# Kernel optimization log

Measured on AMD Instinct MI355X. Metric: run time of the kernel, lower is better.

Reference implementation:

```python
import jax, jax.numpy as jnp
import numpy as np

D_MODEL = 1024
D_K = 1024
D_V = 1024
N_HEAD = 16
EPS = 1e-5
BS, N_TOK = 2, 2048


def setup_inputs() -> dict:
    key = jax.random.key(0)
    ks = jax.random.split(key, 12)
    s = 0.02
    q = jax.random.normal(ks[0], (BS, N_TOK, D_MODEL), jnp.float32)
    k = jax.random.normal(ks[1], (BS, N_TOK, D_MODEL), jnp.float32)
    v = jax.random.normal(ks[2], (BS, N_TOK, D_MODEL), jnp.float32)
    return {
        "q": q, "k": k, "v": v,
        "gamma": jnp.ones((D_MODEL,), jnp.float32),
        "beta": jnp.zeros((D_MODEL,), jnp.float32),
        "Wq": jax.random.normal(ks[3], (D_MODEL, D_K), jnp.float32) * s,
        "bq": jnp.zeros((D_K,), jnp.float32),
        "Wk": jax.random.normal(ks[4], (D_MODEL, D_K), jnp.float32) * s,
        "bk": jnp.zeros((D_K,), jnp.float32),
        "Wv": jax.random.normal(ks[5], (D_MODEL, D_V), jnp.float32) * s,
        "bv": jnp.zeros((D_V,), jnp.float32),
        "Wo": jax.random.normal(ks[6], (D_V, D_MODEL), jnp.float32) * s,
        "bo": jnp.zeros((D_MODEL,), jnp.float32),
    }


def reference(q, k, v, gamma, beta, Wq, bq, Wk, bk, Wv, bv, Wo, bo):
    # NOTE: original module ignores k, v args; self-attention over q.
    bs, n_tok, d_m = q.shape
    d_h = D_K // N_HEAD
    temper = float(np.sqrt(d_h))

    # LayerNorm1d over d_model
    mu = jnp.mean(q, axis=-1, keepdims=True)
    var = jnp.var(q, axis=-1, keepdims=True)
    h = (q - mu) / jnp.sqrt(var + EPS) * gamma + beta

    # projections; head split = chunk along feature dim -> [bs, H, T, d_h]
    qh = (h @ Wq + bq).reshape(bs, n_tok, N_HEAD, d_h).transpose(0, 2, 1, 3)
    kh = (h @ Wk + bk).reshape(bs, n_tok, N_HEAD, d_h).transpose(0, 2, 1, 3)
    vh = jax.nn.relu(h @ Wv + bv).reshape(bs, n_tok, N_HEAD, d_h).transpose(0, 2, 1, 3)

    scores = jnp.einsum('bhqd,bhkd->bhqk', qh, kh) / temper
    # dropout before softmax in train mode; identity in eval (deterministic ref)
    attn = jax.nn.softmax(scores, axis=-1)
    o = jnp.einsum('bhqk,bhkd->bhqd', attn, vh)  # [bs, H, T, d_h]

    # faithful to torch: view(bs, n_tok, -1) with NO head transpose (head-major merge)
    merged = o.reshape(bs, n_tok, N_HEAD * d_h)
    out = merged @ Wo + bo + q  # proj + residual
    return out
```

## Files before the change

### kernel.cpp

```cpp
#include <hip/hip_runtime.h>

typedef __bf16 bf16;
typedef __bf16 bf16x8 __attribute__((ext_vector_type(8)));
typedef __bf16 bf16x4 __attribute__((ext_vector_type(4)));
typedef float  f32x4  __attribute__((ext_vector_type(4)));
typedef float  f32x16 __attribute__((ext_vector_type(16)));
typedef unsigned int u32;
typedef u32 u32x4 __attribute__((ext_vector_type(4)));

#define AS1U(p) ((const __attribute__((address_space(1))) unsigned int*)(p))
#define AS3U(p) ((__attribute__((address_space(3))) unsigned int*)(p))

static __device__ __forceinline__ u32 pack2(float a, float b) {
    unsigned short ua = __builtin_bit_cast(unsigned short, (bf16)a);
    unsigned short ub = __builtin_bit_cast(unsigned short, (bf16)b);
    return (u32)ua | ((u32)ub << 16);
}

__global__ void prep_kernel(const float* __restrict__ q,
                            const float* __restrict__ gamma,
                            const float* __restrict__ beta,
                            bf16* __restrict__ h,
                            const float* __restrict__ W0, const float* __restrict__ W1,
                            const float* __restrict__ W2, const float* __restrict__ W3,
                            bf16* __restrict__ D0, bf16* __restrict__ D1,
                            bf16* __restrict__ D2, bf16* __restrict__ D3) {
    __shared__ float tile[32][33];
    __shared__ float ssum[4], ssum2[4];
    const int blk = blockIdx.x;
    const int t = threadIdx.x;
    if (blk < 4096) {
        const float* xr = q + (size_t)blk * 1024;
        float4 v = ((const float4*)xr)[t];
        float s  = v.x + v.y + v.z + v.w;
        float s2 = v.x * v.x + v.y * v.y + v.z * v.z + v.w * v.w;
#pragma unroll
        for (int m = 1; m < 64; m <<= 1) {
            s  += __shfl_xor(s, m, 64);
            s2 += __shfl_xor(s2, m, 64);
        }
        const int wid = t >> 6, lane = t & 63;
        if (lane == 0) { ssum[wid] = s; ssum2[wid] = s2; }
        __syncthreads();
        s  = ssum[0] + ssum[1] + ssum[2] + ssum[3];
        s2 = ssum2[0] + ssum2[1] + ssum2[2] + ssum2[3];
        const float mu  = s * (1.f / 1024.f);
        const float var = s2 * (1.f / 1024.f) - mu * mu;
        const float rs  = rsqrtf(var + 1e-5f);
        float4 g = ((const float4*)gamma)[t];
        float4 b = ((const float4*)beta)[t];
        bf16x4 o;
        o[0] = (bf16)((v.x - mu) * rs * g.x + b.x);
        o[1] = (bf16)((v.y - mu) * rs * g.y + b.y);
        o[2] = (bf16)((v.z - mu) * rs * g.z + b.z);
        o[3] = (bf16)((v.w - mu) * rs * g.w + b.w);
        ((bf16x4*)(h + (size_t)blk * 1024))[t] = o;
    } else {
        const int z = blk - 4096;
        const float* W; bf16* D;
        switch (z >> 10) {
            case 0: W = W0; D = D0; break;
            case 1: W = W1; D = D1; break;
            case 2: W = W2; D = D2; break;
            default: W = W3; D = D3; break;
        }
        const int bi = (z & 1023) >> 5, bj = z & 31;
        const int tx = t & 31, ty = t >> 5;
#pragma unroll
        for (int i = 0; i < 4; i++) {
            tile[ty + i * 8][tx] = W[(size_t)(bi * 32 + ty + i * 8) * 1024 + bj * 32 + tx];
        }
        __syncthreads();
#pragma unroll
        for (int i = 0; i < 4; i++) {
            D[(size_t)(bj * 32 + ty + i * 8) * 1024 + bi * 32 + tx] =
                (bf16)tile[tx][ty + i * 8];
        }
    }
}

template <int EPI>
__global__ void gemm_kernel(const bf16* __restrict__ A, const bf16* __restrict__ BT,
                            int N, int K,
                            bf16* __restrict__ Cb,
                            const float* __restrict__ b0, const float* __restrict__ b1,
                            const float* __restrict__ b2, bf16* __restrict__ Vt,
                            float* __restrict__ Cf, const float* __restrict__ bo,
                            const float* __restrict__ resid) {
    __shared__ bf16 Asm[128][32];
    __shared__ bf16 Bsm[128][32];
    const int tid = threadIdx.x;
    const int lane = tid & 63, wave = tid >> 6;
    const int wr = wave >> 1, wc = wave & 1;
    const int nwg = gridDim.x * gridDim.y;
    const int bid0 = blockIdx.y * gridDim.x + blockIdx.x;
    const int bid = (bid0 & 7) * (nwg >> 3) + (bid0 >> 3);
    const int tileN = (bid % gridDim.x) * 128;
    const int tileM = (bid / gridDim.x) * 128;
    const int row16 = lane & 15, g = lane >> 4;

    f32x4 acc[4][4] = {};

    for (int kt = 0; kt < K; kt += 32) {
#pragma unroll
        for (int i = 0; i < 2; i++) {
            int c = tid + i * 256;
            int r = c >> 2, cb = (c & 3) * 16;
            const char* g_ = (const char*)(A + (size_t)(tileM + r) * K + kt) + cb;
            char* l_ = (char*)&Asm[0][0] + c * 16;
            __builtin_amdgcn_global_load_lds(AS1U(g_), AS3U(l_), 16, 0, 0);
        }
#pragma unroll
        for (int i = 0; i < 2; i++) {
            int c = tid + i * 256;
            int r = c >> 2, cb = (c & 3) * 16;
            const char* g_ = (const char*)(BT + (size_t)(tileN + r) * K + kt) + cb;
            char* l_ = (char*)&Bsm[0][0] + c * 16;
            __builtin_amdgcn_global_load_lds(AS1U(g_), AS3U(l_), 16, 0, 0);
        }
        __syncthreads();
        bf16x8 af[4], bfr[4];
#pragma unroll
        for (int m = 0; m < 4; m++)
            af[m] = *(const bf16x8*)&Asm[wr * 64 + m * 16 + row16][g * 8];
#pragma unroll
        for (int n = 0; n < 4; n++)
            bfr[n] = *(const bf16x8*)&Bsm[wc * 64 + n * 16 + row16][g * 8];
#pragma unroll
        for (int m = 0; m < 4; m++)
#pragma unroll
            for (int n = 0; n < 4; n++)
                acc[m][n] = __builtin_amdgcn_mfma_f32_16x16x32_bf16(af[m], bfr[n],
                                                                   acc[m][n], 0, 0, 0);
        __syncthreads();
    }

    if constexpr (EPI == 0) {
        __shared__ bf16 Ep[4][64][64];
        char* ep = (char*)&Ep[wave][0][0];
        const bool isV = (tileN >= 2048);
        if (!isV) {
#pragma unroll
            for (int n = 0; n < 4; n++) {
                const int cl = n * 16 + row16;
                const int gc = tileN + wc * 64 + cl;
                const float bias = gc < 1024 ? b0[gc] : b1[gc - 1024];
                const float scl = gc < 1024 ? 0.18033688011112042f : 1.f;
#pragma unroll
                for (int m = 0; m < 4; m++)
#pragma unroll
                    for (int j = 0; j < 4; j++) {
                        const int rl = m * 16 + g * 4 + j;
                        const float v = (acc[m][n][j] + bias) * scl;
                        *(bf16*)(ep + rl * 128 + ((cl * 2) ^ ((rl & 7) << 4))) = (bf16)v;
                    }
            }
        } else {
#pragma unroll
            for (int n = 0; n < 4; n++) {
                const int dl = n * 16 + row16;
                const float bias = b2[(tileN - 2048) + wc * 64 + dl];
#pragma unroll
                for (int m = 0; m < 4; m++)
#pragma unroll
                    for (int j = 0; j < 4; j++) {
                        const int tl = m * 16 + g * 4 + j;
                        const float v = fmaxf(acc[m][n][j] + bias, 0.f);
                        *(bf16*)(ep + dl * 128 + ((tl * 2) ^ ((dl & 7) << 4))) = (bf16)v;
                    }
            }
        }
        asm volatile("s_waitcnt lgkmcnt(0)" ::: "memory");
        __builtin_amdgcn_sched_barrier(0);
        if (!isV) {
#pragma unroll
            for (int it = 0; it < 8; it++) {
                const int rl = (lane >> 3) + it * 8;
                const bf16x8 vrow = *(const bf16x8*)(ep + rl * 128 +
                                                     (((lane & 7) * 16) ^ ((rl & 7) << 4)));
                const int gr = tileM + wr * 64 + rl;
                const int gc = tileN + wc * 64 + (lane & 7) * 8;
                *(bf16x8*)&Cb[(size_t)gr * N + gc] = vrow;
            }
        } else {
            const int bb = tileM >> 11;
            const int tbase = (tileM & 2047) + wr * 64 + (lane & 7) * 8;
#pragma unroll
            for (int it = 0; it < 8; it++) {
                const int dl = (lane >> 3) + it * 8;
                const bf16x8 vrow = *(const bf16x8*)(ep + dl * 128 +
                                                     (((lane & 7) * 16) ^ ((dl & 7) << 4)));
                const int gd = (tileN - 2048) + wc * 64 + dl;
                const int hh = gd >> 6, dd = gd & 63;
                *(bf16x8*)&Vt[(((size_t)bb * 16 + hh) * 64 + dd) * 2048 + tbase] = vrow;
            }
        }
    } else {
        __shared__ float Epf[4][64][66];
        float* ep = &Epf[wave][0][0];
#pragma unroll
        for (int n = 0; n < 4; n++) {
            const int cl = n * 16 + row16;
            const float bias = bo[tileN + wc * 64 + cl];
#pragma unroll
            for (int m = 0; m < 4; m++)
#pragma unroll
                for (int j = 0; j < 4; j++) {
                    const int rl = m * 16 + g * 4 + j;
                    ep[rl * 66 + cl] = acc[m][n][j] + bias;
                }
        }
        asm volatile("s_waitcnt lgkmcnt(0)" ::: "memory");
        __builtin_amdgcn_sched_barrier(0);
        const int rl0 = lane >> 4;
        const int cl0 = (lane & 15) * 4;
#pragma unroll
        for (int it = 0; it < 16; it++) {
            const int rl = rl0 + it * 4;
            float4 v = *(const float4*)&ep[rl * 66 + cl0];
            const int gr = tileM + wr * 64 + rl;
            const int gc = tileN + wc * 64 + cl0;
            const float4 rv = *(const float4*)&resid[(size_t)gr * N + gc];
            v.x += rv.x; v.y += rv.y; v.z += rv.z; v.w += rv.w;
            *(float4*)&Cf[(size_t)gr * N + gc] = v;
        }
    }
}

__global__ __launch_bounds__(512, 4)
void attn_kernel(const bf16* __restrict__ qkv, const bf16* __restrict__ Vt,
                 bf16* __restrict__ Obuf) {
    const int bid = blockIdx.x;
    const int swz = (bid & 7) * 64 + (bid >> 3);
    const int bh = swz >> 4, qt = swz & 15;
    const int b = bh >> 4, h = bh & 15;
    const int qbase = qt * 128;
    const int tid = threadIdx.x;
    const int lane = tid & 63, wv = tid >> 6;
    const int half = wv >> 2, qw = wv & 3;
    const int c = lane & 31, p = lane >> 5;

    __shared__ bf16 Kl[2][2][64][64];
    __shared__ bf16 Vl[2][2][64][64];

    const bf16* qrow = qkv + (size_t)(b * 2048 + qbase + qw * 32 + c) * 3072 + h * 64;
    bf16x8 qf[4];
#pragma unroll
    for (int ch = 0; ch < 4; ch++)
        qf[ch] = *(const bf16x8*)(qrow + ch * 16 + p * 8);

    const char* kgbase = (const char*)(qkv + (size_t)b * 2048 * 3072 + 1024 + h * 64)
                         + (size_t)(half * 1024) * 6144;
    const char* vgbase = (const char*)(Vt + (size_t)bh * 64 * 2048) + half * 2048;
    const int ht = tid & 255;
    const char* kgp[2]; const char* vgp[2]; int ldo[2];
#pragma unroll
    for (int i = 0; i < 2; i++) {
        const int cc = ht + i * 256;
        const int srow = cc >> 3;
        const int scol = ((cc & 7) * 16) ^ ((srow & 7) << 4);
        kgp[i] = kgbase + (size_t)srow * 6144 + scol;
        vgp[i] = vgbase + (size_t)srow * 4096 + scol;
        ldo[i] = cc * 16;
    }
    char* kldb = (char*)&Kl[half][0][0][0];
    char* vldb = (char*)&Vl[half][0][0][0];

    auto stage = [&](int t, int slot) {
        const size_t ko = (size_t)t * (64 * 6144);
        const size_t vo = (size_t)t * 128;
        const int sb = slot * 8192;
#pragma unroll
        for (int i = 0; i < 2; i++) {
            __builtin_amdgcn_global_load_lds(AS1U(kgp[i] + ko), AS3U(kldb + sb + ldo[i]), 16, 0, 0);
            __builtin_amdgcn_global_load_lds(AS1U(vgp[i] + vo), AS3U(vldb + sb + ldo[i]), 16, 0, 0);
        }
    };

    f32x16 accO[2] = {};
    f32x16 accL = {};
    const f32x16 z16 = {};
    const u32 one2 = 0x3F803F80u;
    const u32x4 onesw = {one2, one2, one2, one2};
    const bf16x8 onesf = __builtin_bit_cast(bf16x8, onesw);

    auto compute = [&](int slot) {
        const char* Kb = (const char*)&Kl[half][slot][0][0];
        const char* Vb = (const char*)&Vl[half][slot][0][0];
#pragma unroll
        for (int cc = 0; cc < 2; cc++) {
            const int tok = cc * 32 + c;
            const bf16x8 kf0 = *(const bf16x8*)(Kb + tok * 128 + ((0 * 32 + p * 16) ^ ((tok & 7) << 4)));
            f32x16 accT = __builtin_amdgcn_mfma_f32_32x32x16_bf16(kf0, qf[0], z16, 0, 0, 0);
#pragma unroll
            for (int ch = 1; ch < 4; ch++) {
                const bf16x8 kf = *(const bf16x8*)(Kb + tok * 128 +
                                                   ((ch * 32 + p * 16) ^ ((tok & 7) << 4)));
                accT = __builtin_amdgcn_mfma_f32_32x32x16_bf16(kf, qf[ch], accT, 0, 0, 0);
            }
            float pv[16];
#pragma unroll
            for (int r = 0; r < 16; r++) pv[r] = exp2f(accT[r]);
            u32 k01 = pack2(pv[0], pv[1]),  k23 = pack2(pv[2], pv[3]);
            u32 k45 = pack2(pv[4], pv[5]),  k67 = pack2(pv[6], pv[7]);
            u32 k89 = pack2(pv[8], pv[9]),  kab = pack2(pv[10], pv[11]);
            u32 kcd = pack2(pv[12], pv[13]), kef = pack2(pv[14], pv[15]);
            asm("v_permlane32_swap_b32 %0, %1" : "+v"(k45), "+v"(k01));
            asm("v_permlane32_swap_b32 %0, %1" : "+v"(k67), "+v"(k23));
            asm("v_permlane32_swap_b32 %0, %1" : "+v"(kcd), "+v"(k89));
            asm("v_permlane32_swap_b32 %0, %1" : "+v"(kef), "+v"(kab));
            u32x4 w0w = {k01, k23, k45, k67};
            u32x4 w1w = {k89, kab, kcd, kef};
            const bf16x8 pf0 = __builtin_bit_cast(bf16x8, w0w);
            const bf16x8 pf1 = __builtin_bit_cast(bf16x8, w1w);
            accL = __builtin_amdgcn_mfma_f32_32x32x16_bf16(pf0, onesf, accL, 0, 0, 0);
            accL = __builtin_amdgcn_mfma_f32_32x32x16_bf16(pf1, onesf, accL, 0, 0, 0);
#pragma unroll
            for (int dc = 0; dc < 2; dc++) {
                const int rd = dc * 32 + c;
                const int sw = (rd & 7) << 4;
                const bf16x8 vf0 = *(const bf16x8*)(Vb + rd * 128 + ((cc * 64 + p * 16) ^ sw));
                const bf16x8 vf1 = *(const bf16x8*)(Vb + rd * 128 + ((cc * 64 + 32 + p * 16) ^ sw));
                accO[dc] = __builtin_amdgcn_mfma_f32_32x32x16_bf16(pf0, vf0, accO[dc], 0, 0, 0);
                accO[dc] = __builtin_amdgcn_mfma_f32_32x32x16_bf16(pf1, vf1, accO[dc], 0, 0, 0);
            }
        }
    };

#define KV_SYNC() do { \
        asm volatile("s_waitcnt vmcnt(0)" ::: "memory"); \
        __builtin_amdgcn_s_barrier(); \
        asm volatile("" ::: "memory"); \
    } while (0)

    stage(0, 0);
#pragma unroll 1
    for (int t = 0; t < 14; t += 2) {
        KV_SYNC(); stage(t + 1, 1); compute(0);
        KV_SYNC(); stage(t + 2, 0); compute(1);
    }
    KV_SYNC(); stage(15, 1); compute(0);
    KV_SYNC(); compute(1);
#undef KV_SYNC

    __syncthreads();
    float* ex = (float*)&Kl[0][0][0][0];
    const int xb = (qw * 64 + lane) * 49;
    if (half) {
#pragma unroll
        for (int dc = 0; dc < 2; dc++)
#pragma unroll
            for (int r = 0; r < 16; r++) ex[xb + dc * 16 + r] = accO[dc][r];
#pragma unroll
        for (int r = 0; r < 16; r++) ex[xb + 32 + r] = accL[r];
    }
    __syncthreads();
    if (!half) {
#pragma unroll
        for (int dc = 0; dc < 2; dc++)
#pragma unroll
            for (int r = 0; r < 16; r++) accO[dc][r] += ex[xb + dc * 16 + r];
#pragma unroll
        for (int r = 0; r < 16; r++) accL[r] += ex[xb + 32 + r];
        bf16* ob = Obuf + ((size_t)bh * 2048 + qbase + qw * 32) * 64;
#pragma unroll
        for (int r = 0; r < 16; r++) {
            const float inv = 1.f / accL[r];
            const int row = (r & 3) + 8 * (r >> 2) + 4 * p;
            ob[(size_t)row * 64 + c]      = (bf16)(accO[0][r] * inv);
            ob[(size_t)row * 64 + 32 + c] = (bf16)(accO[1][r] * inv);
        }
    }
}

extern "C" void kernel_launch(void* const* d_in, const int* in_sizes, int n_in,
                              void* d_out, int out_size, void* d_ws, size_t ws_size,
                              hipStream_t stream) {
    const float* q     = (const float*)d_in[0];
    const float* gamma = (const float*)d_in[3];
    const float* beta  = (const float*)d_in[4];
    const float* Wq    = (const float*)d_in[5];
    const float* bq    = (const float*)d_in[6];
    const float* Wk    = (const float*)d_in[7];
    const float* bk    = (const float*)d_in[8];
    const float* Wv    = (const float*)d_in[9];
    const float* bv    = (const float*)d_in[10];
    const float* Wo    = (const float*)d_in[11];
    const float* bo    = (const float*)d_in[12];
    float* out = (float*)d_out;

    char* ws = (char*)d_ws;
    bf16* h     = (bf16*)(ws);
    bf16* WcatT = (bf16*)(ws + (8u << 20));
    bf16* WoT   = (bf16*)(ws + (14u << 20));
    bf16* qkv   = (bf16*)(ws + (16u << 20));
    bf16* Obuf  = (bf16*)(ws + (40u << 20));
    bf16* Vtb   = (bf16*)(ws + (48u << 20));

    prep_kernel<<<8192, 256, 0, stream>>>(q, gamma, beta, h,
                                          Wq, Wk, Wv, Wo,
                                          WcatT, WcatT + (size_t)1024 * 1024,
                                          WcatT + (size_t)2048 * 1024, WoT);

    gemm_kernel<0><<<dim3(24, 32), 256, 0, stream>>>(h, WcatT, 3072, 1024,
                                                     qkv, bq, bk, bv, Vtb,
                                                     nullptr, nullptr, nullptr);

    attn_kernel<<<512, 512, 0, stream>>>(qkv, Vtb, Obuf);

    gemm_kernel<1><<<dim3(8, 32), 256, 0, stream>>>(Obuf, WoT, 1024, 1024,
                                                    nullptr, nullptr, nullptr, nullptr, nullptr,
                                                    out, bo, q);
}
```

Measured before the change: 128.1 us.

## Rewrite QKV projection GEMM with 256x256 tiles and double-buffered pipelined loads

Replaces the templated GEMM for the QKV projection with a dedicated kernel that uses 256x256 tiles, 8 waves, and double-buffered LDS. It prefetches the next K slices via direct global-to-LDS loads interleaved with MFMA phases, using an XOR swizzle, raised wave priority during MFMA, and explicit barriers. The goal is to hide global load latency that the old single-buffered loop exposed and to raise operand reuse per tile. The trade-off is a much smaller grid (192 blocks), heavier register use, and a fragile hand-scheduled waitcnt/barrier sequence. The output GEMM is only specialized with constant sizes.

```diff
diff --git a/kernel.cpp b/kernel.cpp
--- a/kernel.cpp
+++ b/kernel.cpp
@@ -79,14 +79,166 @@
     }
 }
 
-template <int EPI>
-__global__ void gemm_kernel(const bf16* __restrict__ A, const bf16* __restrict__ BT,
-                            int N, int K,
-                            bf16* __restrict__ Cb,
-                            const float* __restrict__ b0, const float* __restrict__ b1,
-                            const float* __restrict__ b2, bf16* __restrict__ Vt,
-                            float* __restrict__ Cf, const float* __restrict__ bo,
-                            const float* __restrict__ resid) {
+__global__ __launch_bounds__(512, 2)
+void gemm0_kernel(const bf16* __restrict__ A, const bf16* __restrict__ BT,
+                  bf16* __restrict__ Cb,
+                  const float* __restrict__ b0, const float* __restrict__ b1,
+                  const float* __restrict__ b2, bf16* __restrict__ Vt) {
+    __shared__ char lds[65536];
+    const int tid = threadIdx.x;
+    const int lane = tid & 63, wave = tid >> 6;
+    const int wr = wave >> 2, wc = wave & 3;
+    const int row16 = lane & 15, g = lane >> 4;
+    const int bid0 = blockIdx.y * 12 + blockIdx.x;
+    const int bid = (bid0 & 7) * 24 + (bid0 >> 3);
+    const int tileN = (bid % 12) * 256;
+    const int tileM = (bid / 12) * 256;
+
+    auto stageA = [&](int T) {
+        char* dst = lds + (T & 1) * 16384;
+        const size_t colb = (size_t)T * 64;
+#pragma unroll
+        for (int hf = 0; hf < 2; hf++) {
+            const int row = hf * 128 + (tid >> 2);
+            const char* src = (const char*)A + (size_t)(tileM + row) * 2048 + colb
+                              + (((tid & 3) * 16) ^ ((row & 3) << 4));
+            __builtin_amdgcn_global_load_lds(AS1U(src), AS3U(dst + hf * 8192 + tid * 16), 16, 0, 0);
+        }
+    };
+    auto stageB = [&](int T) {
+        char* dst = lds + 32768 + (T & 1) * 16384;
+        const size_t colb = (size_t)T * 64;
+#pragma unroll
+        for (int hf = 0; hf < 2; hf++) {
+            const int row = hf * 128 + (tid >> 2);
+            const char* src = (const char*)BT + (size_t)(tileN + row) * 2048 + colb
+                              + (((tid & 3) * 16) ^ ((row & 3) << 4));
+            __builtin_amdgcn_global_load_lds(AS1U(src), AS3U(dst + hf * 8192 + tid * 16), 16, 0, 0);
+        }
+    };
+
+    f32x4 acc[8][4] = {};
+    stageA(0); stageB(0); stageB(1);
+
+#pragma unroll 1
+    for (int T = 0; T < 32; ++T) {
+        if (T == 31) { asm volatile("s_waitcnt vmcnt(0)" ::: "memory"); }
+        else         { asm volatile("s_waitcnt vmcnt(2)" ::: "memory"); }
+        __builtin_amdgcn_s_barrier();
+        asm volatile("" ::: "memory");
+        const char* Ab = lds + (T & 1) * 16384;
+        const char* Bb = lds + 32768 + (T & 1) * 16384;
+        bf16x8 bfr[4];
+#pragma unroll
+        for (int n = 0; n < 4; n++) {
+            const int b_r = wc * 64 + n * 16 + row16;
+            bfr[n] = *(const bf16x8*)(Bb + b_r * 64 + ((g * 16) ^ ((b_r & 3) << 4)));
+        }
+        bf16x8 af[4];
+#pragma unroll
+        for (int m = 0; m < 4; m++) {
+            const int a_r = wr * 128 + m * 16 + row16;
+            af[m] = *(const bf16x8*)(Ab + a_r * 64 + ((g * 16) ^ ((a_r & 3) << 4)));
+        }
+        if (T < 31) stageA(T + 1);
+        __builtin_amdgcn_s_barrier();
+        asm volatile("s_waitcnt lgkmcnt(0)" ::: "memory");
+        __builtin_amdgcn_sched_barrier(0);
+        __builtin_amdgcn_s_setprio(1);
+#pragma unroll
+        for (int m = 0; m < 4; m++)
+#pragma unroll
+            for (int n = 0; n < 4; n++)
+                acc[m][n] = __builtin_amdgcn_mfma_f32_16x16x32_bf16(af[m], bfr[n], acc[m][n], 0, 0, 0);
+        __builtin_amdgcn_s_setprio(0);
+        __builtin_amdgcn_s_barrier();
+#pragma unroll
+        for (int m = 0; m < 4; m++) {
+            const int a_r = wr * 128 + (m + 4) * 16 + row16;
+            af[m] = *(const bf16x8*)(Ab + a_r * 64 + ((g * 16) ^ ((a_r & 3) << 4)));
+        }
+        if (T < 30) stageB(T + 2);
+        __builtin_amdgcn_s_barrier();
+        asm volatile("s_waitcnt lgkmcnt(0)" ::: "memory");
+        __builtin_amdgcn_sched_barrier(0);
+        __builtin_amdgcn_s_setprio(1);
+#pragma unroll
+        for (int m = 0; m < 4; m++)
+#pragma unroll
+            for (int n = 0; n < 4; n++)
+                acc[m + 4][n] = __builtin_amdgcn_mfma_f32_16x16x32_bf16(af[m], bfr[n], acc[m + 4][n], 0, 0, 0);
+        __builtin_amdgcn_s_setprio(0);
+        __builtin_amdgcn_s_barrier();
+    }
+
+    char* ep = lds + wave * 8192;
+    const bool isV = (tileN >= 2048);
+#pragma unroll 1
+    for (int pm = 0; pm < 2; pm++) {
+        if (!isV) {
+#pragma unroll
+            for (int n = 0; n < 4; n++) {
+                const int cl = n * 16 + row16;
+                const int gc = tileN + wc * 64 + cl;
+                const float bias = gc < 1024 ? b0[gc] : b1[gc - 1024];
+                const float scl = gc < 1024 ? 0.18033688011112042f : 1.f;
+#pragma unroll
+                for (int m = 0; m < 4; m++)
+#pragma unroll
+                    for (int j = 0; j < 4; j++) {
+                        const int rl = m * 16 + g * 4 + j;
+                        const float v = (acc[pm * 4 + m][n][j] + bias) * scl;
+                        *(bf16*)(ep + rl * 128 + ((cl * 2) ^ ((rl & 7) << 4))) = (bf16)v;
+                    }
+            }
+        } else {
+#pragma unroll
+            for (int n = 0; n < 4; n++) {
+                const int dl = n * 16 + row16;
+                const float bias = b2[(tileN - 2048) + wc * 64 + dl];
+#pragma unroll
+                for (int m = 0; m < 4; m++)
+#pragma unroll
+                    for (int j = 0; j < 4; j++) {
+                        const int tl = m * 16 + g * 4 + j;
+                        const float v = fmaxf(acc[pm * 4 + m][n][j] + bias, 0.f);
+                        *(bf16*)(ep + dl * 128 + ((tl * 2) ^ ((dl & 7) << 4))) = (bf16)v;
+                    }
+            }
+        }
+        asm volatile("s_waitcnt lgkmcnt(0)" ::: "memory");
+        __builtin_amdgcn_sched_barrier(0);
+        if (!isV) {
+#pragma unroll
+            for (int it = 0; it < 8; it++) {
+                const int rl = (lane >> 3) + it * 8;
+                const bf16x8 vrow = *(const bf16x8*)(ep + rl * 128 +
+                                                     (((lane & 7) * 16) ^ ((rl & 7) << 4)));
+                const int gr = tileM + wr * 128 + pm * 64 + rl;
+                const int gc = tileN + wc * 64 + (lane & 7) * 8;
+                *(bf16x8*)&Cb[(size_t)gr * 3072 + gc] = vrow;
+            }
+        } else {
+            const int bb = tileM >> 11;
+            const int tbase = (tileM & 2047) + wr * 128 + pm * 64 + (lane & 7) * 8;
+#pragma unroll
+            for (int it = 0; it < 8; it++) {
+                const int dl = (lane >> 3) + it * 8;
+                const bf16x8 vrow = *(const bf16x8*)(ep + dl * 128 +
+                                                     (((lane & 7) * 16) ^ ((dl & 7) << 4)));
+                const int gd = (tileN - 2048) + wc * 64 + dl;
+                const int hh = gd >> 6, dd = gd & 63;
+                *(bf16x8*)&Vt[(((size_t)bb * 16 + hh) * 64 + dd) * 2048 + tbase] = vrow;
+            }
+        }
+        asm volatile("s_waitcnt lgkmcnt(0)" ::: "memory");
+        __builtin_amdgcn_sched_barrier(0);
+    }
+}
+
+__global__ void gemm1_kernel(const bf16* __restrict__ A, const bf16* __restrict__ BT,
+                             float* __restrict__ Cf, const float* __restrict__ bo,
+                             const float* __restrict__ resid) {
     __shared__ bf16 Asm[128][32];
     __shared__ bf16 Bsm[128][32];
     const int tid = threadIdx.x;
@@ -101,22 +253,20 @@
 
     f32x4 acc[4][4] = {};
 
-    for (int kt = 0; kt < K; kt += 32) {
+    for (int kt = 0; kt < 1024; kt += 32) {
 #pragma unroll
         for (int i = 0; i < 2; i++) {
             int c = tid + i * 256;
             int r = c >> 2, cb = (c & 3) * 16;
-            const char* g_ = (const char*)(A + (size_t)(tileM + r) * K + kt) + cb;
-            char* l_ = (char*)&Asm[0][0] + c * 16;
-            __builtin_amdgcn_global_load_lds(AS1U(g_), AS3U(l_), 16, 0, 0);
+            const char* g_ = (const char*)(A + (size_t)(tileM + r) * 1024 + kt) + cb;
+            __builtin_amdgcn_global_load_lds(AS1U(g_), AS3U((char*)&Asm[0][0] + c * 16), 16, 0, 0);
         }
 #pragma unroll
         for (int i = 0; i < 2; i++) {
             int c = tid + i * 256;
             int r = c >> 2, cb = (c & 3) * 16;
-            const char* g_ = (const char*)(BT + (size_t)(tileN + r) * K + kt) + cb;
-            char* l_ = (char*)&Bsm[0][0] + c * 16;
-            __builtin_amdgcn_global_load_lds(AS1U(g_), AS3U(l_), 16, 0, 0);
+            const char* g_ = (const char*)(BT + (size_t)(tileN + r) * 1024 + kt) + cb;
+            __builtin_amdgcn_global_load_lds(AS1U(g_), AS3U((char*)&Bsm[0][0] + c * 16), 16, 0, 0);
         }
         __syncthreads();
         bf16x8 af[4], bfr[4];
@@ -134,96 +284,33 @@
                                                                    acc[m][n], 0, 0, 0);
         __syncthreads();
     }
-
-    if constexpr (EPI == 0) {
-        __shared__ bf16 Ep[4][64][64];
-        char* ep = (char*)&Ep[wave][0][0];
-        const bool isV = (tileN >= 2048);
-        if (!isV) {
-#pragma unroll
-            for (int n = 0; n < 4; n++) {
-                const int cl = n * 16 + row16;
-                const int gc = tileN + wc * 64 + cl;
-                const float bias = gc < 1024 ? b0[gc] : b1[gc - 1024];
-                const float scl = gc < 1024 ? 0.18033688011112042f : 1.f;
-#pragma unroll
-                for (int m = 0; m < 4; m++)
-#pragma unroll
-                    for (int j = 0; j < 4; j++) {
-                        const int rl = m * 16 + g * 4 + j;
-                        const float v = (acc[m][n][j] + bias) * scl;
-                        *(bf16*)(ep + rl * 128 + ((cl * 2) ^ ((rl & 7) << 4))) = (bf16)v;
-                    }
-            }
-        } else {
-#pragma unroll
-            for (int n = 0; n < 4; n++) {
-                const int dl = n * 16 + row16;
-                const float bias = b2[(tileN - 2048) + wc * 64 + dl];
-#pragma unroll
-                for (int m = 0; m < 4; m++)
-#pragma unroll
-                    for (int j = 0; j < 4; j++) {
-                        const int tl = m * 16 + g * 4 + j;
-                        const float v = fmaxf(acc[m][n][j] + bias, 0.f);
-                        *(bf16*)(ep + dl * 128 + ((tl * 2) ^ ((dl & 7) << 4))) = (bf16)v;
-                    }
-            }
-        }
-        asm volatile("s_waitcnt lgkmcnt(0)" ::: "memory");
-        __builtin_amdgcn_sched_barrier(0);
-        if (!isV) {
-#pragma unroll
-            for (int it = 0; it < 8; it++) {
-                const int rl = (lane >> 3) + it * 8;
-                const bf16x8 vrow = *(const bf16x8*)(ep + rl * 128 +
-                                                     (((lane & 7) * 16) ^ ((rl & 7) << 4)));
-                const int gr = tileM + wr * 64 + rl;
-                const int gc = tileN + wc * 64 + (lane & 7) * 8;
-                *(bf16x8*)&Cb[(size_t)gr * N + gc] = vrow;
-            }
-        } else {
-            const int bb = tileM >> 11;
-            const int tbase = (tileM & 2047) + wr * 64 + (lane & 7) * 8;
-#pragma unroll
-            for (int it = 0; it < 8; it++) {
-                const int dl = (lane >> 3) + it * 8;
-                const bf16x8 vrow = *(const bf16x8*)(ep + dl * 128 +
-                                                     (((lane & 7) * 16) ^ ((dl & 7) << 4)));
-                const int gd = (tileN - 2048) + wc * 64 + dl;
-                const int hh = gd >> 6, dd = gd & 63;
-                *(bf16x8*)&Vt[(((size_t)bb * 16 + hh) * 64 + dd) * 2048 + tbase] = vrow;
-            }
-        }
-    } else {
-        __shared__ float Epf[4][64][66];
-        float* ep = &Epf[wave][0][0];
-#pragma unroll
-        for (int n = 0; n < 4; n++) {
-            const int cl = n * 16 + row16;
-            const float bias = bo[tileN + wc * 64 + cl];
-#pragma unroll
-            for (int m = 0; m < 4; m++)
-#pragma unroll
-                for (int j = 0; j < 4; j++) {
-                    const int rl = m * 16 + g * 4 + j;
-                    ep[rl * 66 + cl] = acc[m][n][j] + bias;
-                }
-        }
-        asm volatile("s_waitcnt lgkmcnt(0)" ::: "memory");
-        __builtin_amdgcn_sched_barrier(0);
-        const int rl0 = lane >> 4;
-        const int cl0 = (lane & 15) * 4;
-#pragma unroll
-        for (int it = 0; it < 16; it++) {
-            const int rl = rl0 + it * 4;
-            float4 v = *(const float4*)&ep[rl * 66 + cl0];
-            const int gr = tileM + wr * 64 + rl;
-            const int gc = tileN + wc * 64 + cl0;
-            const float4 rv = *(const float4*)&resid[(size_t)gr * N + gc];
-            v.x += rv.x; v.y += rv.y; v.z += rv.z; v.w += rv.w;
-            *(float4*)&Cf[(size_t)gr * N + gc] = v;
-        }
+    __shared__ float Epf[4][64][66];
+    float* ep = &Epf[wave][0][0];
+#pragma unroll
+    for (int n = 0; n < 4; n++) {
+        const int cl = n * 16 + row16;
+        const float bias = bo[tileN + wc * 64 + cl];
+#pragma unroll
+        for (int m = 0; m < 4; m++)
+#pragma unroll
+            for (int j = 0; j < 4; j++) {
+                const int rl = m * 16 + g * 4 + j;
+                ep[rl * 66 + cl] = acc[m][n][j] + bias;
+            }
+    }
+    asm volatile("s_waitcnt lgkmcnt(0)" ::: "memory");
+    __builtin_amdgcn_sched_barrier(0);
+    const int rl0 = lane >> 4;
+    const int cl0 = (lane & 15) * 4;
+#pragma unroll
+    for (int it = 0; it < 16; it++) {
+        const int rl = rl0 + it * 4;
+        float4 v = *(const float4*)&ep[rl * 66 + cl0];
+        const int gr = tileM + wr * 64 + rl;
+        const int gc = tileN + wc * 64 + cl0;
+        const float4 rv = *(const float4*)&resid[(size_t)gr * 1024 + gc];
+        v.x += rv.x; v.y += rv.y; v.z += rv.z; v.w += rv.w;
+        *(float4*)&Cf[(size_t)gr * 1024 + gc] = v;
     }
 }
 
@@ -290,7 +377,7 @@
 #pragma unroll
         for (int cc = 0; cc < 2; cc++) {
             const int tok = cc * 32 + c;
-            const bf16x8 kf0 = *(const bf16x8*)(Kb + tok * 128 + ((0 * 32 + p * 16) ^ ((tok & 7) << 4)));
+            const bf16x8 kf0 = *(const bf16x8*)(Kb + tok * 128 + ((p * 16) ^ ((tok & 7) << 4)));
             f32x16 accT = __builtin_amdgcn_mfma_f32_32x32x16_bf16(kf0, qf[0], z16, 0, 0, 0);
 #pragma unroll
             for (int ch = 1; ch < 4; ch++) {
@@ -402,13 +489,9 @@
                                           WcatT, WcatT + (size_t)1024 * 1024,
                                           WcatT + (size_t)2048 * 1024, WoT);
 
-    gemm_kernel<0><<<dim3(24, 32), 256, 0, stream>>>(h, WcatT, 3072, 1024,
-                                                     qkv, bq, bk, bv, Vtb,
-                                                     nullptr, nullptr, nullptr);
+    gemm0_kernel<<<dim3(12, 16), 512, 0, stream>>>(h, WcatT, qkv, bq, bk, bv, Vtb);
 
     attn_kernel<<<512, 512, 0, stream>>>(qkv, Vtb, Obuf);
 
-    gemm_kernel<1><<<dim3(8, 32), 256, 0, stream>>>(Obuf, WoT, 1024, 1024,
-                                                    nullptr, nullptr, nullptr, nullptr, nullptr,
-                                                    out, bo, q);
-}
+    gemm1_kernel<<<dim3(8, 32), 256, 0, stream>>>(Obuf, WoT, out, bo, q);
+}
```

Result: slower. 154.1 us (+20.3%).

## Double-buffer QKV GEMM K-loop with prefetch and shared LDS epilogue

Applied to the files above, without the earlier changes.

Splits the templated GEMM into two kernels. The QKV-projection GEMM gets a two-slot LDS ring that prefetches the next K tile while the current one is multiplied, with one barrier per iteration instead of two. It also reuses the staging LDS for the epilogue, sets launch bounds of two blocks per CU, and raises wave priority around the MFMA block. The intent is to hide global-load latency behind compute and cut synchronisation. The output GEMM is only specialised to compile-time sizes.

```diff
diff --git a/kernel.cpp b/kernel.cpp
--- a/kernel.cpp
+++ b/kernel.cpp
@@ -79,14 +79,128 @@
     }
 }
 
-template <int EPI>
-__global__ void gemm_kernel(const bf16* __restrict__ A, const bf16* __restrict__ BT,
-                            int N, int K,
-                            bf16* __restrict__ Cb,
-                            const float* __restrict__ b0, const float* __restrict__ b1,
-                            const float* __restrict__ b2, bf16* __restrict__ Vt,
-                            float* __restrict__ Cf, const float* __restrict__ bo,
-                            const float* __restrict__ resid) {
+__global__ __launch_bounds__(256, 2)
+void gemm0_kernel(const bf16* __restrict__ A, const bf16* __restrict__ BT,
+                  bf16* __restrict__ Cb,
+                  const float* __restrict__ b0, const float* __restrict__ b1,
+                  const float* __restrict__ b2, bf16* __restrict__ Vt) {
+    __shared__ char lds[32768];
+    const int tid = threadIdx.x;
+    const int lane = tid & 63, wave = tid >> 6;
+    const int wr = wave >> 1, wc = wave & 1;
+    const int bid0 = blockIdx.y * 24 + blockIdx.x;
+    const int bid = (bid0 & 7) * 96 + (bid0 >> 3);
+    const int tileN = (bid % 24) * 128;
+    const int tileM = (bid / 24) * 128;
+    const int row16 = lane & 15, g = lane >> 4;
+
+    auto stage = [&](int T, int slot) {
+        const int kt = T * 32;
+        char* ab = lds + slot * 8192;
+        char* bb = lds + 16384 + slot * 8192;
+#pragma unroll
+        for (int i = 0; i < 2; i++) {
+            const int c = tid + i * 256;
+            const int r = c >> 2, cbyte = (c & 3) * 16;
+            const char* ga = (const char*)(A + (size_t)(tileM + r) * 1024 + kt) + cbyte;
+            __builtin_amdgcn_global_load_lds(AS1U(ga), AS3U(ab + c * 16), 16, 0, 0);
+            const char* gb = (const char*)(BT + (size_t)(tileN + r) * 1024 + kt) + cbyte;
+            __builtin_amdgcn_global_load_lds(AS1U(gb), AS3U(bb + c * 16), 16, 0, 0);
+        }
+    };
+
+    f32x4 acc[4][4] = {};
+    stage(0, 0);
+
+#pragma unroll 1
+    for (int T = 0; T < 32; ++T) {
+        asm volatile("s_waitcnt vmcnt(0)" ::: "memory");
+        __builtin_amdgcn_s_barrier();
+        asm volatile("" ::: "memory");
+        if (T < 31) stage(T + 1, (T + 1) & 1);
+        const char* Ab = lds + (T & 1) * 8192;
+        const char* Bb = lds + 16384 + (T & 1) * 8192;
+        bf16x8 af[4], bfr[4];
+#pragma unroll
+        for (int m = 0; m < 4; m++)
+            af[m] = *(const bf16x8*)(Ab + (size_t)(wr * 64 + m * 16 + row16) * 64 + g * 16);
+#pragma unroll
+        for (int n = 0; n < 4; n++)
+            bfr[n] = *(const bf16x8*)(Bb + (size_t)(wc * 64 + n * 16 + row16) * 64 + g * 16);
+        __builtin_amdgcn_s_setprio(1);
+#pragma unroll
+        for (int m = 0; m < 4; m++)
+#pragma unroll
+            for (int n = 0; n < 4; n++)
+                acc[m][n] = __builtin_amdgcn_mfma_f32_16x16x32_bf16(af[m], bfr[n],
+                                                                   acc[m][n], 0, 0, 0);
+        __builtin_amdgcn_s_setprio(0);
+    }
+
+    __syncthreads();
+    char* ep = lds + wave * 8192;
+    const bool isV = (tileN >= 2048);
+    if (!isV) {
+#pragma unroll
+        for (int n = 0; n < 4; n++) {
+            const int cl = n * 16 + row16;
+            const int gc = tileN + wc * 64 + cl;
+            const float bias = gc < 1024 ? b0[gc] : b1[gc - 1024];
+            const float scl = gc < 1024 ? 0.18033688011112042f : 1.f;
+#pragma unroll
+            for (int m = 0; m < 4; m++)
+#pragma unroll
+                for (int j = 0; j < 4; j++) {
+                    const int rl = m * 16 + g * 4 + j;
+                    const float v = (acc[m][n][j] + bias) * scl;
+                    *(bf16*)(ep + rl * 128 + ((cl * 2) ^ ((rl & 7) << 4))) = (bf16)v;
+                }
+        }
+    } else {
+#pragma unroll
+        for (int n = 0; n < 4; n++) {
+            const int dl = n * 16 + row16;
+            const float bias = b2[(tileN - 2048) + wc * 64 + dl];
+#pragma unroll
+            for (int m = 0; m < 4; m++)
+#pragma unroll
+                for (int j = 0; j < 4; j++) {
+                    const int tl = m * 16 + g * 4 + j;
+                    const float v = fmaxf(acc[m][n][j] + bias, 0.f);
+                    *(bf16*)(ep + dl * 128 + ((tl * 2) ^ ((dl & 7) << 4))) = (bf16)v;
+                }
+        }
+    }
+    asm volatile("s_waitcnt lgkmcnt(0)" ::: "memory");
+    __builtin_amdgcn_sched_barrier(0);
+    if (!isV) {
+#pragma unroll
+        for (int it = 0; it < 8; it++) {
+            const int rl = (lane >> 3) + it * 8;
+            const bf16x8 vrow = *(const bf16x8*)(ep + rl * 128 +
+                                                 (((lane & 7) * 16) ^ ((rl & 7) << 4)));
+            const int gr = tileM + wr * 64 + rl;
+            const int gc = tileN + wc * 64 + (lane & 7) * 8;
+            *(bf16x8*)&Cb[(size_t)gr * 3072 + gc] = vrow;
+        }
+    } else {
+        const int bb = tileM >> 11;
+        const int tbase = (tileM & 2047) + wr * 64 + (lane & 7) * 8;
+#pragma unroll
+        for (int it = 0; it < 8; it++) {
+            const int dl = (lane >> 3) + it * 8;
+            const bf16x8 vrow = *(const bf16x8*)(ep + dl * 128 +
+                                                 (((lane & 7) * 16) ^ ((dl & 7) << 4)));
+            const int gd = (tileN - 2048) + wc * 64 + dl;
+            const int hh = gd >> 6, dd = gd & 63;
+            *(bf16x8*)&Vt[(((size_t)bb * 16 + hh) * 64 + dd) * 2048 + tbase] = vrow;
+        }
+    }
+}
+
+__global__ void gemm1_kernel(const bf16* __restrict__ A, const bf16* __restrict__ BT,
+                             float* __restrict__ Cf, const float* __restrict__ bo,
+                             const float* __restrict__ resid) {
     __shared__ bf16 Asm[128][32];
     __shared__ bf16 Bsm[128][32];
     const int tid = threadIdx.x;
@@ -101,22 +215,20 @@
 
     f32x4 acc[4][4] = {};
 
-    for (int kt = 0; kt < K; kt += 32) {
+    for (int kt = 0; kt < 1024; kt += 32) {
 #pragma unroll
         for (int i = 0; i < 2; i++) {
             int c = tid + i * 256;
             int r = c >> 2, cb = (c & 3) * 16;
-            const char* g_ = (const char*)(A + (size_t)(tileM + r) * K + kt) + cb;
-            char* l_ = (char*)&Asm[0][0] + c * 16;
-            __builtin_amdgcn_global_load_lds(AS1U(g_), AS3U(l_), 16, 0, 0);
+            const char* g_ = (const char*)(A + (size_t)(tileM + r) * 1024 + kt) + cb;
+            __builtin_amdgcn_global_load_lds(AS1U(g_), AS3U((char*)&Asm[0][0] + c * 16), 16, 0, 0);
         }
 #pragma unroll
         for (int i = 0; i < 2; i++) {
             int c = tid + i * 256;
             int r = c >> 2, cb = (c & 3) * 16;
-            const char* g_ = (const char*)(BT + (size_t)(tileN + r) * K + kt) + cb;
-            char* l_ = (char*)&Bsm[0][0] + c * 16;
-            __builtin_amdgcn_global_load_lds(AS1U(g_), AS3U(l_), 16, 0, 0);
+            const char* g_ = (const char*)(BT + (size_t)(tileN + r) * 1024 + kt) + cb;
+            __builtin_amdgcn_global_load_lds(AS1U(g_), AS3U((char*)&Bsm[0][0] + c * 16), 16, 0, 0);
         }
         __syncthreads();
         bf16x8 af[4], bfr[4];
@@ -134,96 +246,33 @@
                                                                    acc[m][n], 0, 0, 0);
         __syncthreads();
     }
-
-    if constexpr (EPI == 0) {
-        __shared__ bf16 Ep[4][64][64];
-        char* ep = (char*)&Ep[wave][0][0];
-        const bool isV = (tileN >= 2048);
-        if (!isV) {
-#pragma unroll
-            for (int n = 0; n < 4; n++) {
-                const int cl = n * 16 + row16;
-                const int gc = tileN + wc * 64 + cl;
-                const float bias = gc < 1024 ? b0[gc] : b1[gc - 1024];
-                const float scl = gc < 1024 ? 0.18033688011112042f : 1.f;
-#pragma unroll
-                for (int m = 0; m < 4; m++)
-#pragma unroll
-                    for (int j = 0; j < 4; j++) {
-                        const int rl = m * 16 + g * 4 + j;
-                        const float v = (acc[m][n][j] + bias) * scl;
-                        *(bf16*)(ep + rl * 128 + ((cl * 2) ^ ((rl & 7) << 4))) = (bf16)v;
-                    }
+    __shared__ float Epf[4][64][66];
+    float* ep = &Epf[wave][0][0];
+#pragma unroll
+    for (int n = 0; n < 4; n++) {
+        const int cl = n * 16 + row16;
+        const float bias = bo[tileN + wc * 64 + cl];
+#pragma unroll
+        for (int m = 0; m < 4; m++)
+#pragma unroll
+            for (int j = 0; j < 4; j++) {
+                const int rl = m * 16 + g * 4 + j;
+                ep[rl * 66 + cl] = acc[m][n][j] + bias;
             }
-        } else {
-#pragma unroll
-            for (int n = 0; n < 4; n++) {
-                const int dl = n * 16 + row16;
-                const float bias = b2[(tileN - 2048) + wc * 64 + dl];
-#pragma unroll
-                for (int m = 0; m < 4; m++)
-#pragma unroll
-                    for (int j = 0; j < 4; j++) {
-                        const int tl = m * 16 + g * 4 + j;
-                        const float v = fmaxf(acc[m][n][j] + bias, 0.f);
-                        *(bf16*)(ep + dl * 128 + ((tl * 2) ^ ((dl & 7) << 4))) = (bf16)v;
-                    }
-            }
-        }
-        asm volatile("s_waitcnt lgkmcnt(0)" ::: "memory");
-        __builtin_amdgcn_sched_barrier(0);
-        if (!isV) {
-#pragma unroll
-            for (int it = 0; it < 8; it++) {
-                const int rl = (lane >> 3) + it * 8;
-                const bf16x8 vrow = *(const bf16x8*)(ep + rl * 128 +
-                                                     (((lane & 7) * 16) ^ ((rl & 7) << 4)));
-                const int gr = tileM + wr * 64 + rl;
-                const int gc = tileN + wc * 64 + (lane & 7) * 8;
-                *(bf16x8*)&Cb[(size_t)gr * N + gc] = vrow;
-            }
-        } else {
-            const int bb = tileM >> 11;
-            const int tbase = (tileM & 2047) + wr * 64 + (lane & 7) * 8;
-#pragma unroll
-            for (int it = 0; it < 8; it++) {
-                const int dl = (lane >> 3) + it * 8;
-                const bf16x8 vrow = *(const bf16x8*)(ep + dl * 128 +
-                                                     (((lane & 7) * 16) ^ ((dl & 7) << 4)));
-                const int gd = (tileN - 2048) + wc * 64 + dl;
-                const int hh = gd >> 6, dd = gd & 63;
-                *(bf16x8*)&Vt[(((size_t)bb * 16 + hh) * 64 + dd) * 2048 + tbase] = vrow;
-            }
-        }
-    } else {
-        __shared__ float Epf[4][64][66];
-        float* ep = &Epf[wave][0][0];
-#pragma unroll
-        for (int n = 0; n < 4; n++) {
-            const int cl = n * 16 + row16;
-            const float bias = bo[tileN + wc * 64 + cl];
-#pragma unroll
-            for (int m = 0; m < 4; m++)
-#pragma unroll
-                for (int j = 0; j < 4; j++) {
-                    const int rl = m * 16 + g * 4 + j;
-                    ep[rl * 66 + cl] = acc[m][n][j] + bias;
-                }
-        }
-        asm volatile("s_waitcnt lgkmcnt(0)" ::: "memory");
-        __builtin_amdgcn_sched_barrier(0);
-        const int rl0 = lane >> 4;
-        const int cl0 = (lane & 15) * 4;
-#pragma unroll
-        for (int it = 0; it < 16; it++) {
-            const int rl = rl0 + it * 4;
-            float4 v = *(const float4*)&ep[rl * 66 + cl0];
-            const int gr = tileM + wr * 64 + rl;
-            const int gc = tileN + wc * 64 + cl0;
-            const float4 rv = *(const float4*)&resid[(size_t)gr * N + gc];
-            v.x += rv.x; v.y += rv.y; v.z += rv.z; v.w += rv.w;
-            *(float4*)&Cf[(size_t)gr * N + gc] = v;
-        }
+    }
+    asm volatile("s_waitcnt lgkmcnt(0)" ::: "memory");
+    __builtin_amdgcn_sched_barrier(0);
+    const int rl0 = lane >> 4;
+    const int cl0 = (lane & 15) * 4;
+#pragma unroll
+    for (int it = 0; it < 16; it++) {
+        const int rl = rl0 + it * 4;
+        float4 v = *(const float4*)&ep[rl * 66 + cl0];
+        const int gr = tileM + wr * 64 + rl;
+        const int gc = tileN + wc * 64 + cl0;
+        const float4 rv = *(const float4*)&resid[(size_t)gr * 1024 + gc];
+        v.x += rv.x; v.y += rv.y; v.z += rv.z; v.w += rv.w;
+        *(float4*)&Cf[(size_t)gr * 1024 + gc] = v;
     }
 }
 
@@ -290,7 +339,7 @@
 #pragma unroll
         for (int cc = 0; cc < 2; cc++) {
             const int tok = cc * 32 + c;
-            const bf16x8 kf0 = *(const bf16x8*)(Kb + tok * 128 + ((0 * 32 + p * 16) ^ ((tok & 7) << 4)));
+            const bf16x8 kf0 = *(const bf16x8*)(Kb + tok * 128 + ((p * 16) ^ ((tok & 7) << 4)));
             f32x16 accT = __builtin_amdgcn_mfma_f32_32x32x16_bf16(kf0, qf[0], z16, 0, 0, 0);
 #pragma unroll
             for (int ch = 1; ch < 4; ch++) {
@@ -402,13 +451,9 @@
                                           WcatT, WcatT + (size_t)1024 * 1024,
                                           WcatT + (size_t)2048 * 1024, WoT);
 
-    gemm_kernel<0><<<dim3(24, 32), 256, 0, stream>>>(h, WcatT, 3072, 1024,
-                                                     qkv, bq, bk, bv, Vtb,
-                                                     nullptr, nullptr, nullptr);
+    gemm0_kernel<<<dim3(24, 32), 256, 0, stream>>>(h, WcatT, qkv, bq, bk, bv, Vtb);
 
     attn_kernel<<<512, 512, 0, stream>>>(qkv, Vtb, Obuf);
 
-    gemm_kernel<1><<<dim3(8, 32), 256, 0, stream>>>(Obuf, WoT, 1024, 1024,
-                                                    nullptr, nullptr, nullptr, nullptr, nullptr,
-                                                    out, bo, q);
-}
+    gemm1_kernel<<<dim3(8, 32), 256, 0, stream>>>(Obuf, WoT, out, bo, q);
+}
```

Result: no change. 127.2 us (-0.7%).
